# Kernel tuning notes

Hardware: AMD Instinct MI355X
Metric: run time of the kernel (lower is better)

The kernel has to match this reference:

```python
import jax, jax.numpy as jnp
import numpy as np

EMBED_DIM = 512
N_HEADS = 8
HEAD_DIM = EMBED_DIM // N_HEADS
B, S = 4, 2048

def gelu(x):
    # torch F.gelu default = exact erf gelu
    return jax.nn.gelu(x, approximate=False)

def setup_inputs() -> dict:
    key = jax.random.key(0)
    ks = jax.random.split(key, 9)
    sc = 1.0 / np.sqrt(EMBED_DIM)
    inp = {
        'x':   jax.random.normal(ks[0], (B, S, EMBED_DIM), dtype=jnp.float32),
        'Wq':  jax.random.uniform(ks[1], (EMBED_DIM, EMBED_DIM), jnp.float32, -sc, sc),
        'bq':  jax.random.uniform(ks[2], (EMBED_DIM,), jnp.float32, -sc, sc),
        'Wk':  jax.random.uniform(ks[3], (EMBED_DIM, EMBED_DIM), jnp.float32, -sc, sc),
        'bk':  jax.random.uniform(ks[4], (EMBED_DIM,), jnp.float32, -sc, sc),
        'Wv':  jax.random.uniform(ks[5], (EMBED_DIM, EMBED_DIM), jnp.float32, -sc, sc),
        'bv':  jax.random.uniform(ks[6], (EMBED_DIM,), jnp.float32, -sc, sc),
        'Wo':  jax.random.uniform(ks[7], (EMBED_DIM, EMBED_DIM), jnp.float32, -sc, sc),
        'bo':  jax.random.uniform(ks[8], (EMBED_DIM,), jnp.float32, -sc, sc),
    }
    return inp

def reference(x, Wq, bq, Wk, bk, Wv, bv, Wo, bo):
    Bsz, Ssz, _ = x.shape
    def proj(W, b):
        # [B,S,E] -> [B,H,S,D], GELU applied before head split (same math either way)
        h = gelu(jnp.einsum('bse,ef->bsf', x, W.T) + b)
        return h.reshape(Bsz, Ssz, N_HEADS, HEAD_DIM).transpose(0, 2, 1, 3)
    q = proj(Wq, bq)
    k = proj(Wk, bk)
    v = proj(Wv, bv)
    attn = jnp.einsum('bhid,bhjd->bhij', q, k) / np.sqrt(HEAD_DIM).astype(np.float32)
    attn = jax.nn.softmax(attn, axis=-1)
    o = jnp.einsum('bhij,bhjd->bhid', attn, v)
    o = o.transpose(0, 2, 1, 3).reshape(Bsz, Ssz, EMBED_DIM)
    return gelu(jnp.einsum('bse,ef->bsf', o, Wo.T) + bo)
```

## Files before the change

kernel.cpp:

```cpp
#include <hip/hip_runtime.h>
#include <hip/hip_bf16.h>

typedef __bf16 bf16_t;
typedef __bf16 bf16x4 __attribute__((ext_vector_type(4)));
typedef __bf16 bf16x8 __attribute__((ext_vector_type(8)));
typedef float  f32x4  __attribute__((ext_vector_type(4)));
typedef float  f32x8  __attribute__((ext_vector_type(8)));
typedef unsigned int u32;
typedef u32 u32x4 __attribute__((ext_vector_type(4)));

#define EMBED 512
#define NH    8
#define HD    64
#define SEQ   2048
#define MTOT  8192
#define SCQ   0.18033688011112042f

__device__ __forceinline__ float gelu_f(float x) {
    return 0.5f * x * (1.0f + erff(x * 0.7071067811865475f));
}

__device__ __forceinline__ f32x4 mfma16(bf16x8 a, bf16x8 b, f32x4 c) {
    return __builtin_amdgcn_mfma_f32_16x16x32_bf16(a, b, c, 0, 0, 0);
}

__device__ __forceinline__ void barrier_nodrain() {
    asm volatile("s_waitcnt lgkmcnt(0)" ::: "memory");
    __builtin_amdgcn_s_barrier();
    asm volatile("" ::: "memory");
}

__device__ __forceinline__ u32 cvtpk_bf16(float lo, float hi) {
    u32 r;
    asm("v_cvt_pk_bf16_f32 %0, %1, %2" : "=v"(r) : "v"(lo), "v"(hi));
    return r;
}
__device__ __forceinline__ void swap32(u32& a, u32& b) {
    asm volatile("v_permlane32_swap_b32 %0, %1" : "+v"(a), "+v"(b));
}
__device__ __forceinline__ void swap16(u32& a, u32& b) {
    asm volatile("v_permlane16_swap_b32 %0, %1" : "+v"(a), "+v"(b));
}

template<int MODE, int NTILE>
__global__ __launch_bounds__(256, 3)
void gemm_gelu_kernel(const void*  __restrict__ Xp,
                      const float* __restrict__ W0, const float* __restrict__ W1,
                      const float* __restrict__ W2,
                      const float* __restrict__ Bq, const float* __restrict__ Bk,
                      const float* __restrict__ Bv,
                      bf16_t* __restrict__ O0, bf16_t* __restrict__ O1,
                      bf16_t* __restrict__ O2, float* __restrict__ Of)
{
    constexpr int NTN = NTILE / 32;
    __shared__ __align__(16) bf16_t As[128 * 72];
    __shared__ __align__(16) bf16_t Bs[NTILE * 72];
    const int tid  = threadIdx.x;
    const int lane = tid & 63, w = tid >> 6, quad = lane >> 4, l15 = lane & 15;
    const int m0 = blockIdx.x * 128;
    int mat, n0;
    if (MODE == 0) { mat = blockIdx.y >> 2; n0 = (blockIdx.y & 3) * NTILE; }
    else           { mat = 0;               n0 = blockIdx.y * NTILE; }
    const float* W  = (MODE == 0) ? (mat == 0 ? W0 : (mat == 1 ? W1 : W2)) : W0;
    const float* Bi = (MODE == 1) ? Bq : (mat == 0 ? Bq : (mat == 1 ? Bk : Bv));
    const float*  Xf = (const float*)Xp;
    const bf16_t* Xb = (const bf16_t*)Xp;

    const int wr = (w >> 1) * 64;
    const int wc = (w & 1) * (NTILE / 2);

    const int srow = tid >> 3, scol = (tid & 7) * 8;

    f32x4 acc[4][NTN];
#pragma unroll
    for (int a = 0; a < 4; ++a)
#pragma unroll
        for (int b = 0; b < NTN; ++b) acc[a][b] = f32x4{0.f, 0.f, 0.f, 0.f};

    f32x8  xpf[4];
    bf16x8 xpb[4];

#pragma unroll
    for (int it = 0; it < 4; ++it) {
        const size_t r = (size_t)(m0 + it * 32 + srow);
        if (MODE == 0) xpf[it] = *(const f32x8*)(Xf + r * EMBED + scol);
        else           xpb[it] = *(const bf16x8*)(Xb + r * EMBED + scol);
    }

#pragma unroll 1
    for (int kt = 0; kt < 8; ++kt) {
        const int k0 = kt * 64;
        barrier_nodrain();
#pragma unroll
        for (int it = 0; it < 4; ++it) {
            if (MODE == 0)
                *(bf16x8*)(As + (it * 32 + srow) * 72 + scol) =
                    __builtin_convertvector(xpf[it], bf16x8);
            else
                *(bf16x8*)(As + (it * 32 + srow) * 72 + scol) = xpb[it];
        }
#pragma unroll
        for (int it = 0; it < NTN; ++it) {
            const int r = it * 32 + srow;
            const f32x8 wv = *(const f32x8*)(W + (size_t)(n0 + r) * EMBED + k0 + scol);
            *(bf16x8*)(Bs + r * 72 + scol) = __builtin_convertvector(wv, bf16x8);
        }
        if (kt < 7) {
            const int k1 = k0 + 64;
#pragma unroll
            for (int it = 0; it < 4; ++it) {
                const size_t r = (size_t)(m0 + it * 32 + srow);
                if (MODE == 0) xpf[it] = *(const f32x8*)(Xf + r * EMBED + k1 + scol);
                else           xpb[it] = *(const bf16x8*)(Xb + r * EMBED + k1 + scol);
            }
        }
        barrier_nodrain();
#pragma unroll
        for (int ks = 0; ks < 2; ++ks) {
            const int ko = (ks * 4 + quad) * 8;
            bf16x8 av[4], bv[NTN];
#pragma unroll
            for (int mt = 0; mt < 4; ++mt)
                av[mt] = *(const bf16x8*)(As + (wr + mt * 16 + l15) * 72 + ko);
#pragma unroll
            for (int nt = 0; nt < NTN; ++nt)
                bv[nt] = *(const bf16x8*)(Bs + (wc + nt * 16 + l15) * 72 + ko);
#pragma unroll
            for (int mt = 0; mt < 4; ++mt)
#pragma unroll
                for (int nt = 0; nt < NTN; ++nt)
                    acc[mt][nt] = mfma16(av[mt], bv[nt], acc[mt][nt]);
        }
    }

    float biasv[NTN];
#pragma unroll
    for (int nt = 0; nt < NTN; ++nt)
        biasv[nt] = Bi[n0 + wc + nt * 16 + l15];
#pragma unroll
    for (int mt = 0; mt < 4; ++mt) {
        const int mb = m0 + wr + mt * 16 + quad * 4;
        const int bb = mb >> 11, s0 = mb & (SEQ - 1);
#pragma unroll
        for (int nt = 0; nt < NTN; ++nt) {
            const int fc = n0 + wc + nt * 16 + l15;
            const int h = fc >> 6, d = fc & 63;
            float vv[4];
#pragma unroll
            for (int i = 0; i < 4; ++i) vv[i] = gelu_f(acc[mt][nt][i] + biasv[nt]);
            if (MODE == 1) {
#pragma unroll
                for (int i = 0; i < 4; ++i) Of[(size_t)(mb + i) * EMBED + fc] = vv[i];
            } else if (mat == 0) {
#pragma unroll
                for (int i = 0; i < 4; ++i)
                    O0[(((size_t)(bb * NH + h)) * SEQ + s0 + i) * HD + d] = (bf16_t)(vv[i] * SCQ);
            } else if (mat == 1) {
#pragma unroll
                for (int i = 0; i < 4; ++i)
                    O1[(((size_t)(bb * NH + h)) * SEQ + s0 + i) * HD + d] = (bf16_t)vv[i];
            } else {
                bf16x4 pk;
#pragma unroll
                for (int i = 0; i < 4; ++i) pk[i] = (bf16_t)vv[i];
                *(bf16x4*)(O2 + ((size_t)(bb * NH + h) * HD + d) * SEQ + s0) = pk;
            }
        }
    }
}

#define FA_ITER(T, BUF, KR0, KR1, VR0, VR1)                                   \
    do {                                                                      \
        if ((T) + 1 < 32) {                                                   \
            bf16_t* Kn = Ks[(BUF) ^ 1];                                       \
            bf16_t* Vn = Vs[(BUF) ^ 1];                                       \
            *(bf16x8*)(Kn + sA)        = KR0;                                 \
            *(bf16x8*)(Kn + sA + 2048) = KR1;                                 \
            *(bf16x8*)(Vn + sA)        = VR0;                                 \
            *(bf16x8*)(Vn + sA + 2048) = VR1;                                 \
        }                                                                     \
        if ((T) + 3 < 32) {                                                   \
            const int kv = ((T) + 3) * 64;                                    \
            KR0 = *(const bf16x8*)(K + baseQK + (size_t)(kv + r0) * HD + c0); \
            KR1 = *(const bf16x8*)(K + baseQK + (size_t)(kv + r0 + 32) * HD + c0); \
            VR0 = *(const bf16x8*)(Vt + baseV + (size_t)r0 * SEQ + kv + c0);  \
            VR1 = *(const bf16x8*)(Vt + baseV + (size_t)(r0 + 32) * SEQ + kv + c0); \
        }                                                                     \
        const bf16_t* Kb = Ks[(BUF)];                                         \
        const bf16_t* Vb = Vs[(BUF)];                                         \
        f32x4 sf[4];                                                          \
        _Pragma("unroll")                                                     \
        for (int jt = 0; jt < 4; ++jt) sf[jt] = f32x4{0.f, 0.f, 0.f, 0.f};    \
        __builtin_amdgcn_s_setprio(1);                                        \
        _Pragma("unroll")                                                     \
        for (int ks = 0; ks < 2; ++ks) {                                      \
            const int ko = (ks * 32 + quad * 8) ^ cx;                         \
            _Pragma("unroll")                                                 \
            for (int jt = 0; jt < 4; ++jt) {                                  \
                const bf16x8 a = *(const bf16x8*)(Kb + ((jt * 16 + l15) << 6) + ko); \
                sf[jt] = mfma16(a, qf[ks], sf[jt]);                           \
            }                                                                 \
        }                                                                     \
        __builtin_amdgcn_s_setprio(0);                                        \
        u32 w0[4], w1[4];                                                     \
        _Pragma("unroll")                                                     \
        for (int jt = 0; jt < 4; ++jt) {                                      \
            _Pragma("unroll")                                                 \
            for (int i = 0; i < 4; ++i) sf[jt][i] = exp2f(sf[jt][i]);         \
            lacc += sf[jt];                                                   \
            w0[jt] = cvtpk_bf16(sf[jt][0], sf[jt][1]);                        \
            w1[jt] = cvtpk_bf16(sf[jt][2], sf[jt][3]);                        \
        }                                                                     \
        swap32(w0[0], w0[1]); swap16(w0[0], w0[1]);                           \
        swap32(w1[0], w1[1]); swap16(w1[0], w1[1]);                           \
        swap32(w0[2], w0[3]); swap16(w0[2], w0[3]);                           \
        swap32(w1[2], w1[3]); swap16(w1[2], w1[3]);                           \
        const u32x4 pq0 = u32x4{w0[0], w1[0], w0[1], w1[1]};                  \
        const u32x4 pq1 = u32x4{w0[2], w1[2], w0[3], w1[3]};                  \
        const bf16x8 pa0 = __builtin_bit_cast(bf16x8, pq0);                   \
        const bf16x8 pa1 = __builtin_bit_cast(bf16x8, pq1);                   \
        __builtin_amdgcn_s_setprio(1);                                        \
        _Pragma("unroll")                                                     \
        for (int c = 0; c < 2; ++c) {                                         \
            const int ko = (c * 32 + quad * 8) ^ cx;                          \
            const bf16x8 pa = c ? pa1 : pa0;                                  \
            _Pragma("unroll")                                                 \
            for (int nt = 0; nt < 4; ++nt) {                                  \
                const bf16x8 b = *(const bf16x8*)(Vb + ((nt * 16 + l15) << 6) + ko); \
                oacc[nt] = mfma16(pa, b, oacc[nt]);                           \
            }                                                                 \
        }                                                                     \
        __builtin_amdgcn_s_setprio(0);                                        \
        if ((T) < 31) barrier_nodrain();                                      \
    } while (0)

__global__ __launch_bounds__(256, 4)
void flash_attn_kernel(const bf16_t* __restrict__ Q,
                       const bf16_t* __restrict__ K,
                       const bf16_t* __restrict__ Vt,
                       bf16_t* __restrict__ Og)
{
    __shared__ __align__(16) bf16_t Ks[2][64 * 64];
    __shared__ __align__(16) bf16_t Vs[2][64 * 64];

    const int tid  = threadIdx.x;
    const int lane = tid & 63, w = tid >> 6, quad = lane >> 4, l15 = lane & 15;
    const int bh = blockIdx.y;
    const int q0 = blockIdx.x * 64;
    const size_t baseQK = (size_t)bh * SEQ * HD;
    const size_t baseV  = (size_t)bh * HD * SEQ;
    const int wm = w * 16;
    const int cx = (l15 & 7) << 3;

    bf16x8 qf[2];
#pragma unroll
    for (int ks = 0; ks < 2; ++ks)
        qf[ks] = *(const bf16x8*)(Q + baseQK + (size_t)(q0 + wm + l15) * HD + ks * 32 + quad * 8);

    f32x4 lacc = f32x4{0.f, 0.f, 0.f, 0.f};
    f32x4 oacc[4];
#pragma unroll
    for (int nt = 0; nt < 4; ++nt) oacc[nt] = f32x4{0.f, 0.f, 0.f, 0.f};

    const int r0 = tid >> 3, c0 = (tid & 7) * 8;
    const int sA = (r0 << 6) + (c0 ^ ((r0 & 7) << 3));

    bf16x8 kA0, kA1, vA0, vA1;
    bf16x8 kB0, kB1, vB0, vB1;

    kA0 = *(const bf16x8*)(K + baseQK + (size_t)r0 * HD + c0);
    kA1 = *(const bf16x8*)(K + baseQK + (size_t)(r0 + 32) * HD + c0);
    vA0 = *(const bf16x8*)(Vt + baseV + (size_t)r0 * SEQ + c0);
    vA1 = *(const bf16x8*)(Vt + baseV + (size_t)(r0 + 32) * SEQ + c0);
    *(bf16x8*)(Ks[0] + sA)        = kA0;
    *(bf16x8*)(Ks[0] + sA + 2048) = kA1;
    *(bf16x8*)(Vs[0] + sA)        = vA0;
    *(bf16x8*)(Vs[0] + sA + 2048) = vA1;
    kB0 = *(const bf16x8*)(K + baseQK + (size_t)(64 + r0) * HD + c0);
    kB1 = *(const bf16x8*)(K + baseQK + (size_t)(64 + r0 + 32) * HD + c0);
    vB0 = *(const bf16x8*)(Vt + baseV + (size_t)r0 * SEQ + 64 + c0);
    vB1 = *(const bf16x8*)(Vt + baseV + (size_t)(r0 + 32) * SEQ + 64 + c0);
    kA0 = *(const bf16x8*)(K + baseQK + (size_t)(128 + r0) * HD + c0);
    kA1 = *(const bf16x8*)(K + baseQK + (size_t)(128 + r0 + 32) * HD + c0);
    vA0 = *(const bf16x8*)(Vt + baseV + (size_t)r0 * SEQ + 128 + c0);
    vA1 = *(const bf16x8*)(Vt + baseV + (size_t)(r0 + 32) * SEQ + 128 + c0);
    barrier_nodrain();

#pragma unroll 1
    for (int tt = 0; tt < 32; tt += 2) {
        FA_ITER(tt,     0, kB0, kB1, vB0, vB1);
        FA_ITER(tt + 1, 1, kA0, kA1, vA0, vA1);
    }

    const int bidx = bh >> 3, h = bh & 7;
    float rs = (lacc[0] + lacc[1]) + (lacc[2] + lacc[3]);
    rs += __shfl_xor(rs, 16);
    rs += __shfl_xor(rs, 32);
    float lf[4];
#pragma unroll
    for (int i = 0; i < 4; ++i)
        lf[i] = __shfl(rs, (lane & 48) | (quad * 4 + i));
#pragma unroll
    for (int nt = 0; nt < 4; ++nt)
#pragma unroll
        for (int i = 0; i < 4; ++i) {
            const int s = q0 + wm + quad * 4 + i;
            const int d = nt * 16 + l15;
            Og[((size_t)(bidx * SEQ + s)) * EMBED + h * HD + d] =
                (bf16_t)(oacc[nt][i] / lf[i]);
        }
}

extern "C" void kernel_launch(void* const* d_in, const int* in_sizes, int n_in,
                              void* d_out, int out_size, void* d_ws, size_t ws_size,
                              hipStream_t stream)
{
    const float* x  = (const float*)d_in[0];
    const float* Wq = (const float*)d_in[1];
    const float* bq = (const float*)d_in[2];
    const float* Wk = (const float*)d_in[3];
    const float* bk = (const float*)d_in[4];
    const float* Wv = (const float*)d_in[5];
    const float* bv = (const float*)d_in[6];
    const float* Wo = (const float*)d_in[7];
    const float* bo = (const float*)d_in[8];
    float* out = (float*)d_out;

    const size_t NE = (size_t)MTOT * EMBED;
    bf16_t* Qw  = (bf16_t*)d_out + NE;
    bf16_t* Kw  = (bf16_t*)d_ws;
    bf16_t* Vtw = Kw + NE;
    bf16_t* Ow  = Vtw + NE;

    gemm_gelu_kernel<0, 128><<<dim3(64, 12), 256, 0, stream>>>(
        x, Wq, Wk, Wv, bq, bk, bv, Qw, Kw, Vtw, nullptr);
    flash_attn_kernel<<<dim3(32, 32), 256, 0, stream>>>(Qw, Kw, Vtw, Ow);
    gemm_gelu_kernel<1, 64><<<dim3(64, 8), 256, 0, stream>>>(
        Ow, Wo, nullptr, nullptr, bo, nullptr, nullptr,
        nullptr, nullptr, nullptr, out);
}
```

Measured before the change: 179.4 us.

## Fuse QKV GEMM, attention and output GEMM into one persistent kernel

The three launches (QKV projection GEMM, flash attention, output GEMM) become a single persistent kernel of 512 blocks. The blocks step through the tiles of each stage and meet at a software grid barrier built from atomics. The barrier counter sits in the first 8 bytes of the output buffer and is zeroed by a memset before launch. This is meant to remove inter-kernel launch gaps and tail drain. In exchange, occupancy is capped at 2 blocks per CU, and the tile counts per stage no longer divide evenly across the blocks.

```diff
diff --git a/kernel.cpp b/kernel.cpp
--- a/kernel.cpp
+++ b/kernel.cpp
@@ -15,6 +15,7 @@
 #define SEQ   2048
 #define MTOT  8192
 #define SCQ   0.18033688011112042f
+#define NBLK  512
 
 __device__ __forceinline__ float gelu_f(float x) {
     return 0.5f * x * (1.0f + erff(x * 0.7071067811865475f));
@@ -42,25 +43,42 @@
     asm volatile("v_permlane16_swap_b32 %0, %1" : "+v"(a), "+v"(b));
 }
 
+__device__ __forceinline__ void gbar(u32* bar) {
+    __threadfence();
+    __syncthreads();
+    if (threadIdx.x == 0) {
+        const u32 g = atomicAdd(&bar[1], 0u);
+        const u32 v = atomicAdd(&bar[0], 1u);
+        if (v == NBLK - 1u) {
+            atomicExch(&bar[0], 0u);
+            __threadfence();
+            atomicAdd(&bar[1], 1u);
+        } else {
+            while (atomicAdd(&bar[1], 0u) == g) __builtin_amdgcn_s_sleep(2);
+        }
+    }
+    __syncthreads();
+    __threadfence();
+}
+
 template<int MODE, int NTILE>
-__global__ __launch_bounds__(256, 3)
-void gemm_gelu_kernel(const void*  __restrict__ Xp,
-                      const float* __restrict__ W0, const float* __restrict__ W1,
-                      const float* __restrict__ W2,
-                      const float* __restrict__ Bq, const float* __restrict__ Bk,
-                      const float* __restrict__ Bv,
-                      bf16_t* __restrict__ O0, bf16_t* __restrict__ O1,
-                      bf16_t* __restrict__ O2, float* __restrict__ Of)
+__device__ __forceinline__
+void gemm_body(int bx, int by, const void* __restrict__ Xp,
+               const float* __restrict__ W0, const float* __restrict__ W1,
+               const float* __restrict__ W2,
+               const float* __restrict__ Bq, const float* __restrict__ Bk,
+               const float* __restrict__ Bv,
+               bf16_t* __restrict__ O0, bf16_t* __restrict__ O1,
+               bf16_t* __restrict__ O2, float* __restrict__ Of,
+               bf16_t* As, bf16_t* Bs)
 {
     constexpr int NTN = NTILE / 32;
-    __shared__ __align__(16) bf16_t As[128 * 72];
-    __shared__ __align__(16) bf16_t Bs[NTILE * 72];
     const int tid  = threadIdx.x;
     const int lane = tid & 63, w = tid >> 6, quad = lane >> 4, l15 = lane & 15;
-    const int m0 = blockIdx.x * 128;
+    const int m0 = bx * 128;
     int mat, n0;
-    if (MODE == 0) { mat = blockIdx.y >> 2; n0 = (blockIdx.y & 3) * NTILE; }
-    else           { mat = 0;               n0 = blockIdx.y * NTILE; }
+    if (MODE == 0) { mat = by >> 2; n0 = (by & 3) * NTILE; }
+    else           { mat = 0;       n0 = by * NTILE; }
     const float* W  = (MODE == 0) ? (mat == 0 ? W0 : (mat == 1 ? W1 : W2)) : W0;
     const float* Bi = (MODE == 1) ? Bq : (mat == 0 ? Bq : (mat == 1 ? Bk : Bv));
     const float*  Xf = (const float*)Xp;
@@ -68,7 +86,6 @@
 
     const int wr = (w >> 1) * 64;
     const int wc = (w & 1) * (NTILE / 2);
-
     const int srow = tid >> 3, scol = (tid & 7) * 8;
 
     f32x4 acc[4][NTN];
@@ -79,7 +96,6 @@
 
     f32x8  xpf[4];
     bf16x8 xpb[4];
-
 #pragma unroll
     for (int it = 0; it < 4; ++it) {
         const size_t r = (size_t)(m0 + it * 32 + srow);
@@ -172,8 +188,8 @@
 #define FA_ITER(T, BUF, KR0, KR1, VR0, VR1)                                   \
     do {                                                                      \
         if ((T) + 1 < 32) {                                                   \
-            bf16_t* Kn = Ks[(BUF) ^ 1];                                       \
-            bf16_t* Vn = Vs[(BUF) ^ 1];                                       \
+            bf16_t* Kn = KS + (((BUF) ^ 1) << 12);                            \
+            bf16_t* Vn = VS + (((BUF) ^ 1) << 12);                            \
             *(bf16x8*)(Kn + sA)        = KR0;                                 \
             *(bf16x8*)(Kn + sA + 2048) = KR1;                                 \
             *(bf16x8*)(Vn + sA)        = VR0;                                 \
@@ -186,8 +202,8 @@
             VR0 = *(const bf16x8*)(Vt + baseV + (size_t)r0 * SEQ + kv + c0);  \
             VR1 = *(const bf16x8*)(Vt + baseV + (size_t)(r0 + 32) * SEQ + kv + c0); \
         }                                                                     \
-        const bf16_t* Kb = Ks[(BUF)];                                         \
-        const bf16_t* Vb = Vs[(BUF)];                                         \
+        const bf16_t* Kb = KS + ((BUF) << 12);                                \
+        const bf16_t* Vb = VS + ((BUF) << 12);                                \
         f32x4 sf[4];                                                          \
         _Pragma("unroll")                                                     \
         for (int jt = 0; jt < 4; ++jt) sf[jt] = f32x4{0.f, 0.f, 0.f, 0.f};    \
@@ -234,19 +250,15 @@
         if ((T) < 31) barrier_nodrain();                                      \
     } while (0)
 
-__global__ __launch_bounds__(256, 4)
-void flash_attn_kernel(const bf16_t* __restrict__ Q,
-                       const bf16_t* __restrict__ K,
-                       const bf16_t* __restrict__ Vt,
-                       bf16_t* __restrict__ Og)
+__device__ __forceinline__
+void flash_body(int t, const bf16_t* __restrict__ Q, const bf16_t* __restrict__ K,
+                const bf16_t* __restrict__ Vt, bf16_t* __restrict__ Og,
+                bf16_t* KS, bf16_t* VS)
 {
-    __shared__ __align__(16) bf16_t Ks[2][64 * 64];
-    __shared__ __align__(16) bf16_t Vs[2][64 * 64];
-
     const int tid  = threadIdx.x;
     const int lane = tid & 63, w = tid >> 6, quad = lane >> 4, l15 = lane & 15;
-    const int bh = blockIdx.y;
-    const int q0 = blockIdx.x * 64;
+    const int bh = t >> 5;
+    const int q0 = (t & 31) * 64;
     const size_t baseQK = (size_t)bh * SEQ * HD;
     const size_t baseV  = (size_t)bh * HD * SEQ;
     const int wm = w * 16;
@@ -272,10 +284,10 @@
     kA1 = *(const bf16x8*)(K + baseQK + (size_t)(r0 + 32) * HD + c0);
     vA0 = *(const bf16x8*)(Vt + baseV + (size_t)r0 * SEQ + c0);
     vA1 = *(const bf16x8*)(Vt + baseV + (size_t)(r0 + 32) * SEQ + c0);
-    *(bf16x8*)(Ks[0] + sA)        = kA0;
-    *(bf16x8*)(Ks[0] + sA + 2048) = kA1;
-    *(bf16x8*)(Vs[0] + sA)        = vA0;
-    *(bf16x8*)(Vs[0] + sA + 2048) = vA1;
+    *(bf16x8*)(KS + sA)        = kA0;
+    *(bf16x8*)(KS + sA + 2048) = kA1;
+    *(bf16x8*)(VS + sA)        = vA0;
+    *(bf16x8*)(VS + sA + 2048) = vA1;
     kB0 = *(const bf16x8*)(K + baseQK + (size_t)(64 + r0) * HD + c0);
     kB1 = *(const bf16x8*)(K + baseQK + (size_t)(64 + r0 + 32) * HD + c0);
     vB0 = *(const bf16x8*)(Vt + baseV + (size_t)r0 * SEQ + 64 + c0);
@@ -309,6 +321,38 @@
             Og[((size_t)(bidx * SEQ + s)) * EMBED + h * HD + d] =
                 (bf16_t)(oacc[nt][i] / lf[i]);
         }
+}
+
+__global__ __launch_bounds__(256, 2)
+void mega_kernel(const float* __restrict__ x,
+                 const float* __restrict__ Wq, const float* __restrict__ bq,
+                 const float* __restrict__ Wk, const float* __restrict__ bk,
+                 const float* __restrict__ Wv, const float* __restrict__ bv,
+                 const float* __restrict__ Wo, const float* __restrict__ bo,
+                 float* __restrict__ out,
+                 bf16_t* __restrict__ Qw, bf16_t* __restrict__ Kw,
+                 bf16_t* __restrict__ Vtw, bf16_t* __restrict__ Ow,
+                 u32* __restrict__ bar)
+{
+    __shared__ __align__(16) char smem[36864];
+    bf16_t* As = (bf16_t*)smem;
+    bf16_t* Bs = As + 128 * 72;
+    bf16_t* KS = (bf16_t*)smem;
+    bf16_t* VS = KS + 8192;
+
+    const int bid = blockIdx.x;
+
+    for (int t = bid; t < 768; t += NBLK)
+        gemm_body<0, 128>(t & 63, t >> 6, x, Wq, Wk, Wv, bq, bk, bv,
+                          Qw, Kw, Vtw, nullptr, As, Bs);
+    gbar(bar);
+
+    for (int t = bid; t < 1024; t += NBLK)
+        flash_body(t, Qw, Kw, Vtw, Ow, KS, VS);
+    gbar(bar);
+
+    gemm_body<1, 64>(bid & 63, bid >> 6, Ow, Wo, nullptr, nullptr,
+                     bo, nullptr, nullptr, nullptr, nullptr, nullptr, out, As, Bs);
 }
 
 extern "C" void kernel_launch(void* const* d_in, const int* in_sizes, int n_in,
@@ -331,11 +375,9 @@
     bf16_t* Kw  = (bf16_t*)d_ws;
     bf16_t* Vtw = Kw + NE;
     bf16_t* Ow  = Vtw + NE;
-
-    gemm_gelu_kernel<0, 128><<<dim3(64, 12), 256, 0, stream>>>(
-        x, Wq, Wk, Wv, bq, bk, bv, Qw, Kw, Vtw, nullptr);
-    flash_attn_kernel<<<dim3(32, 32), 256, 0, stream>>>(Qw, Kw, Vtw, Ow);
-    gemm_gelu_kernel<1, 64><<<dim3(64, 8), 256, 0, stream>>>(
-        Ow, Wo, nullptr, nullptr, bo, nullptr, nullptr,
-        nullptr, nullptr, nullptr, out);
-}
+    u32*    bar = (u32*)d_out;
+
+    hipMemsetAsync(bar, 0, 8, stream);
+    mega_kernel<<<dim3(NBLK), dim3(256), 0, stream>>>(
+        x, Wq, bq, Wk, bk, Wv, bv, Wo, bo, out, Qw, Kw, Vtw, Ow, bar);
+}
```

Result: slower. 428.9 us (+139.1%).
